# Performance work log

Measured on AMD Instinct MI355X. Metric: run time of the kernel, lower is better.

The kernel has to match this reference:

```python
import jax, jax.numpy as jnp
import numpy as np

N_NODES = 50000
N_EDGES = 800000
D_IN = 96
HID = 128


def _glorot(key, shape):
    fan_in, fan_out = shape[0], shape[1]
    lim = np.sqrt(6.0 / (fan_in + fan_out)).astype(np.float32)
    return jax.random.uniform(key, shape, jnp.float32, -lim, lim)


def setup_inputs() -> dict:
    key = jax.random.key(0)
    ks = jax.random.split(key, 12)
    x = jax.random.normal(ks[0], (N_NODES, D_IN), jnp.float32)
    edge_index = jax.random.randint(ks[1], (2, N_EDGES), 0, N_NODES)
    return {
        "x": x,
        "edge_index": edge_index,
        "W_in": _glorot(ks[2], (D_IN, HID)),
        "b_in": jnp.zeros((HID,), jnp.float32),
        "W1": _glorot(ks[3], (HID, HID)),
        "b1": jnp.zeros((HID,), jnp.float32),
        "W2": _glorot(ks[4], (HID, HID)),
        "b2": jnp.zeros((HID,), jnp.float32),
        "Wm1": _glorot(ks[5], (2 * HID, HID)),
        "bm1": jnp.zeros((HID,), jnp.float32),
        "Wm2": _glorot(ks[6], (HID, 1)),
        "bm2": jnp.zeros((1,), jnp.float32),
    }


def _gcn_conv(h, W, b, src, dst, n_nodes):
    # PyG GCNConv with add_self_loops=True, normalize=True:
    # out = D^{-1/2} (A + I) D^{-1/2} (h W) + b, aggregating x_j (source) into dst.
    loop = jnp.arange(n_nodes)
    row = jnp.concatenate([src, loop])  # source / j
    col = jnp.concatenate([dst, loop])  # target / i
    deg = jax.ops.segment_sum(jnp.ones(row.shape, h.dtype), col, num_segments=n_nodes)
    dinv = jnp.where(deg > 0, jax.lax.rsqrt(deg), 0.0)
    norm = dinv[row] * dinv[col]  # [E+N]
    xw = h @ W  # [N, H]
    msg = xw[row] * norm[:, None]  # gather + scale, [E+N, H]
    out = jax.ops.segment_sum(msg, col, num_segments=n_nodes)  # scatter-add
    return out + b


def reference(x, edge_index, W_in, b_in, W1, b1, W2, b2, Wm1, bm1, Wm2, bm2):
    src, dst = edge_index[0], edge_index[1]
    n = x.shape[0]
    h = jax.nn.relu(x @ W_in + b_in)  # dropout is identity at inference
    h = jax.nn.relu(_gcn_conv(h, W1, b1, src, dst, n))
    h = jax.nn.relu(_gcn_conv(h, W2, b2, src, dst, n))
    ef = jnp.concatenate([h[src], h[dst]], axis=1)  # [E, 2H]
    hid = jax.nn.relu(ef @ Wm1 + bm1)
    logits = (hid @ Wm2 + bm2)[:, 0]  # [E]
    return logits
```

## Files before the change

### kernel.cpp

```cpp
#include <hip/hip_runtime.h>

#define N_NODES 50000
#define N_EDGES 800000
#define D_IN 96
#define HID 128
#define NB 391
#define BCAP 3072

typedef __attribute__((ext_vector_type(8))) _Float16 halfx8;
typedef __attribute__((ext_vector_type(2))) _Float16 half2v;
typedef __attribute__((ext_vector_type(16))) float f32x16;


__global__ __launch_bounds__(256) void bucket_hist_kernel(const int* __restrict__ dst,
                                                          int* __restrict__ bhist) {
    __shared__ int lh[NB];
    int t = threadIdx.x;
    for (int i = t; i < NB; i += 256) lh[i] = 0;
    __syncthreads();
    int base = blockIdx.x * 4096;
#pragma unroll
    for (int i = 0; i < 16; i++) {
        int e = base + i * 256 + t;
        if (e < N_EDGES) atomicAdd(&lh[dst[e] >> 7], 1);
    }
    __syncthreads();
    for (int i = t; i < NB; i += 256) atomicAdd(&bhist[i], lh[i]);
}

__global__ __launch_bounds__(512) void scan_buckets_kernel(const int* __restrict__ bhist,
                                                           int* __restrict__ boff,
                                                           int* __restrict__ bcursor) {
    __shared__ int s[512];
    int t = threadIdx.x;
    int v = (t < NB) ? bhist[t] : 0;
    s[t] = v;
    __syncthreads();
    for (int off = 1; off < 512; off <<= 1) {
        int u = (t >= off) ? s[t - off] : 0;
        __syncthreads();
        s[t] += u;
        __syncthreads();
    }
    if (t < NB) {
        int ex = s[t] - v;
        boff[t] = ex;
        bcursor[t] = ex;
    }
    if (t == NB - 1) boff[NB] = s[t];
}

__global__ __launch_bounds__(512) void bin_kernel(const int* __restrict__ src,
                                                  const int* __restrict__ dst,
                                                  int* __restrict__ bcursor,
                                                  unsigned long long* __restrict__ binned) {
    __shared__ int lh[NB];
    __shared__ int gbs[NB];
    int t = threadIdx.x;
    for (int i = t; i < NB; i += 512) lh[i] = 0;
    __syncthreads();
    int base = blockIdx.x * 8192;
    unsigned long long pk[16];
    int bb[16], rk[16];
#pragma unroll
    for (int i = 0; i < 16; i++) {
        int e = base + i * 512 + t;
        bb[i] = -1;
        if (e < N_EDGES) {
            int s = src[e], d = dst[e];
            int b = d >> 7;
            bb[i] = b;
            pk[i] = ((unsigned long long)s << 27) |
                    ((unsigned long long)(d & 127) << 20) | (unsigned long long)e;
            rk[i] = atomicAdd(&lh[b], 1);
        }
    }
    __syncthreads();
    for (int i = t; i < NB; i += 512) gbs[i] = atomicAdd(&bcursor[i], lh[i]);
    __syncthreads();
#pragma unroll
    for (int i = 0; i < 16; i++) {
        if (bb[i] >= 0) binned[gbs[bb[i]] + rk[i]] = pk[i];
    }
}

__global__ __launch_bounds__(256) void bucket_sort_kernel(const unsigned long long* __restrict__ binned,
                                                          const int* __restrict__ boff,
                                                          int2* __restrict__ ce_se,
                                                          int* __restrict__ ce_dst,
                                                          int* __restrict__ csr_ptr,
                                                          float* __restrict__ dinv) {
    __shared__ unsigned long long ed[BCAP];
    __shared__ int2 sorted[BCAP];
    __shared__ int cntA[128], sc[128];
    int b = blockIdx.x;
    int t = threadIdx.x;
    int base = boff[b];
    int k = boff[b + 1] - base;
    if (k > BCAP) k = BCAP;
    if (t < 128) { cntA[t] = 0; }
    __syncthreads();
    int rk[12], li[12];
    int nmine = 0;
    for (int i = t; i < k; i += 256) {
        unsigned long long p = binned[base + i];
        ed[i] = p;
        int d = (int)((p >> 20) & 127);
        rk[nmine] = atomicAdd(&cntA[d], 1);
        li[nmine] = i;
        nmine++;
    }
    __syncthreads();
    if (t < 128) sc[t] = cntA[t];
    __syncthreads();
    for (int off = 1; off < 128; off <<= 1) {
        int u = 0;
        if (t < 128 && t >= off) u = sc[t - off];
        __syncthreads();
        if (t < 128) sc[t] += u;
        __syncthreads();
    }
    for (int m = 0; m < nmine; m++) {
        unsigned long long p = ed[li[m]];
        int d = (int)((p >> 20) & 127);
        int pos = sc[d] - cntA[d] + rk[m];
        int srcn = (int)(p >> 27);
        int eid = (int)(p & 0xFFFFF);
        sorted[pos] = make_int2(srcn | (d << 16), eid);
    }
    __syncthreads();
    for (int i = t; i < k; i += 256) {
        int2 se = sorted[i];
        ce_se[base + i] = make_int2(se.x & 0xFFFF, se.y);
        ce_dst[base + i] = (b << 7) + (se.x >> 16);
    }
    if (t < 128) {
        int node = (b << 7) + t;
        if (node < N_NODES) {
            csr_ptr[node] = base + sc[t] - cntA[t];
            dinv[node] = 1.0f / sqrtf((float)(cntA[t] + 1));
        }
    }
    if (b == NB - 1 && t == 0) csr_ptr[N_NODES] = boff[NB];
}

__global__ __launch_bounds__(256) void convert_x_kernel(const float* __restrict__ x,
                                                        _Float16* __restrict__ xh, int n4) {
    int i = blockIdx.x * 256 + threadIdx.x;
    if (i < n4) {
        float4 v = ((const float4*)x)[i];
        half2v a = {(_Float16)v.x, (_Float16)v.y};
        half2v b = {(_Float16)v.z, (_Float16)v.w};
        ((half2v*)xh)[i * 2] = a;
        ((half2v*)xh)[i * 2 + 1] = b;
    }
}

__global__ __launch_bounds__(256) void pack_weights_kernel(const float* __restrict__ W_in,
                                                           const float* __restrict__ W1,
                                                           const float* __restrict__ W2,
                                                           const float* __restrict__ Wm1,
                                                           _Float16* __restrict__ packed) {
    int t = blockIdx.x * 256 + threadIdx.x;
    const float* Wsrc;
    int K, u;
    if (t < 12288)      { Wsrc = W_in;            K = 96;  u = t; }
    else if (t < 28672) { Wsrc = W1;              K = 128; u = t - 12288; }
    else if (t < 45056) { Wsrc = W2;              K = 128; u = t - 28672; }
    else if (t < 61440) { Wsrc = Wm1;             K = 128; u = t - 45056; }
    else                { Wsrc = Wm1 + 128 * 128; K = 128; u = t - 61440; }
    if (t >= 77824) return;
    int steps = K >> 4;
    int cb = u / (steps * 512);
    int rem = u - cb * steps * 512;
    int s = rem >> 9;
    int lane = (rem >> 3) & 63;
    int j = rem & 7;
    int k = s * 16 + ((lane >> 5) << 3) + j;
    int n = (cb << 5) + (lane & 31);
    packed[t] = (_Float16)Wsrc[k * 128 + n];
}

__global__ __launch_bounds__(256) void gemm_f16_kernel(const _Float16* __restrict__ A,
                                                       const _Float16* __restrict__ Wp,
                                                       const float* __restrict__ bias,
                                                       const float* __restrict__ rowscale,
                                                       _Float16* __restrict__ out,
                                                       int M, int K, int steps, int dorelu) {
    __shared__ _Float16 As[64 * 136];
    int tid = threadIdx.x;
    int M0 = blockIdx.x * 64;
    int stride = K + 8;
    int CH = K >> 3;
    int tot = 64 * CH;
    for (int i = tid; i < tot; i += 256) {
        int r = i / CH, c = i - r * CH;
        uint4 v = make_uint4(0, 0, 0, 0);
        int row = M0 + r;
        if (row < M) v = *(const uint4*)&A[(size_t)row * K + c * 8];
        *(uint4*)&As[r * stride + c * 8] = v;
    }
    __syncthreads();

    int wave = tid >> 6, lane = tid & 63;
    int rb = wave & 1;
    int cb0 = (wave >> 1) * 2;
    const halfx8* bp0 = (const halfx8*)Wp + (size_t)cb0 * steps * 64 + lane;
    const halfx8* bp1 = bp0 + (size_t)steps * 64;
    const _Float16* arow = &As[(rb * 32 + (lane & 31)) * stride + ((lane >> 5) << 3)];
    f32x16 acc0 = {}, acc1 = {};
    for (int s = 0; s < steps; s++) {
        halfx8 a = *(const halfx8*)&arow[s * 16];
        halfx8 b0 = bp0[s * 64];
        halfx8 b1 = bp1[s * 64];
        acc0 = __builtin_amdgcn_mfma_f32_32x32x16_f16(a, b0, acc0, 0, 0, 0);
        acc1 = __builtin_amdgcn_mfma_f32_32x32x16_f16(a, b1, acc1, 0, 0, 0);
    }

    int colA = cb0 * 32 + (lane & 31);
    int colB = colA + 32;
    float bA = bias ? bias[colA] : 0.f;
    float bB = bias ? bias[colB] : 0.f;
#pragma unroll
    for (int r = 0; r < 16; r++) {
        int rl = (r & 3) + 8 * (r >> 2) + 4 * (lane >> 5);
        int grow = M0 + rb * 32 + rl;
        if (grow < M) {
            float sc = rowscale ? rowscale[grow] : 1.f;
            float v0 = (acc0[r] + bA) * sc;
            float v1 = (acc1[r] + bB) * sc;
            if (dorelu) { v0 = fmaxf(v0, 0.f); v1 = fmaxf(v1, 0.f); }
            out[(size_t)grow * 128 + colA] = (_Float16)v0;
            out[(size_t)grow * 128 + colB] = (_Float16)v1;
        }
    }
}

__global__ __launch_bounds__(256) void gemm_uv_kernel(const _Float16* __restrict__ A,
                                                      const _Float16* __restrict__ WpU,
                                                      const _Float16* __restrict__ WpV,
                                                      const float* __restrict__ bm1,
                                                      _Float16* __restrict__ U,
                                                      _Float16* __restrict__ V,
                                                      int M) {
    const int K = 128, steps = 8;
    __shared__ _Float16 As[64 * 136];
    int tid = threadIdx.x;
    int M0 = blockIdx.x * 64;
    int stride = K + 8;
    for (int i = tid; i < 64 * 16; i += 256) {
        int r = i >> 4, c = i & 15;
        uint4 v = make_uint4(0, 0, 0, 0);
        int row = M0 + r;
        if (row < M) v = *(const uint4*)&A[(size_t)row * K + c * 8];
        *(uint4*)&As[r * stride + c * 8] = v;
    }
    __syncthreads();

    int wave = tid >> 6, lane = tid & 63;
    int rb = wave & 1;
    int cb0 = (wave >> 1) * 2;
    const halfx8* bu0 = (const halfx8*)WpU + (size_t)cb0 * steps * 64 + lane;
    const halfx8* bu1 = bu0 + (size_t)steps * 64;
    const halfx8* bv0 = (const halfx8*)WpV + (size_t)cb0 * steps * 64 + lane;
    const halfx8* bv1 = bv0 + (size_t)steps * 64;
    const _Float16* arow = &As[(rb * 32 + (lane & 31)) * stride + ((lane >> 5) << 3)];
    f32x16 au0 = {}, au1 = {}, av0 = {}, av1 = {};
    for (int s = 0; s < steps; s++) {
        halfx8 a = *(const halfx8*)&arow[s * 16];
        au0 = __builtin_amdgcn_mfma_f32_32x32x16_f16(a, bu0[s * 64], au0, 0, 0, 0);
        au1 = __builtin_amdgcn_mfma_f32_32x32x16_f16(a, bu1[s * 64], au1, 0, 0, 0);
        av0 = __builtin_amdgcn_mfma_f32_32x32x16_f16(a, bv0[s * 64], av0, 0, 0, 0);
        av1 = __builtin_amdgcn_mfma_f32_32x32x16_f16(a, bv1[s * 64], av1, 0, 0, 0);
    }

    int colA = cb0 * 32 + (lane & 31);
    int colB = colA + 32;
    float bA = bm1[colA], bB = bm1[colB];
#pragma unroll
    for (int r = 0; r < 16; r++) {
        int rl = (r & 3) + 8 * (r >> 2) + 4 * (lane >> 5);
        int grow = M0 + rb * 32 + rl;
        if (grow < M) {
            U[(size_t)grow * 128 + colA] = (_Float16)(au0[r] + bA);
            U[(size_t)grow * 128 + colB] = (_Float16)(au1[r] + bB);
            V[(size_t)grow * 128 + colA] = (_Float16)av0[r];
            V[(size_t)grow * 128 + colB] = (_Float16)av1[r];
        }
    }
}

__global__ __launch_bounds__(256) void aggregate_kernel(const _Float16* __restrict__ y,
                                                        const float* __restrict__ dinv,
                                                        const int* __restrict__ ptr,
                                                        const int2* __restrict__ ce_se,
                                                        const float* __restrict__ bias,
                                                        _Float16* __restrict__ out) {
    int node = blockIdx.x * 4 + (threadIdx.x >> 6);
    int lane = threadIdx.x & 63;
    int c = lane * 2;
    float di = dinv[node];
    half2v self = ((const half2v*)&y[(size_t)node * 128])[lane];
    float a0 = (float)self.x, a1 = (float)self.y;
    float b0 = 0.f, b1 = 0.f, c0 = 0.f, c1 = 0.f, d0 = 0.f, d1 = 0.f;
    int s0 = ptr[node], s1 = ptr[node + 1];
    int j = s0;
    for (; j + 7 < s1; j += 8) {
        int n0 = ce_se[j].x, n1 = ce_se[j + 1].x, n2 = ce_se[j + 2].x, n3 = ce_se[j + 3].x;
        int n4 = ce_se[j + 4].x, n5 = ce_se[j + 5].x, n6 = ce_se[j + 6].x, n7 = ce_se[j + 7].x;
        half2v v0 = ((const half2v*)&y[(size_t)n0 * 128])[lane];
        half2v v1 = ((const half2v*)&y[(size_t)n1 * 128])[lane];
        half2v v2 = ((const half2v*)&y[(size_t)n2 * 128])[lane];
        half2v v3 = ((const half2v*)&y[(size_t)n3 * 128])[lane];
        half2v v4 = ((const half2v*)&y[(size_t)n4 * 128])[lane];
        half2v v5 = ((const half2v*)&y[(size_t)n5 * 128])[lane];
        half2v v6 = ((const half2v*)&y[(size_t)n6 * 128])[lane];
        half2v v7 = ((const half2v*)&y[(size_t)n7 * 128])[lane];
        a0 += (float)v0.x + (float)v4.x; a1 += (float)v0.y + (float)v4.y;
        b0 += (float)v1.x + (float)v5.x; b1 += (float)v1.y + (float)v5.y;
        c0 += (float)v2.x + (float)v6.x; c1 += (float)v2.y + (float)v6.y;
        d0 += (float)v3.x + (float)v7.x; d1 += (float)v3.y + (float)v7.y;
    }
    for (; j < s1; j++) {
        int n = ce_se[j].x;
        half2v v = ((const half2v*)&y[(size_t)n * 128])[lane];
        a0 += (float)v.x; a1 += (float)v.y;
    }
    float2 bv = *(const float2*)&bias[c];
    float o0 = fmaxf(di * (a0 + b0 + c0 + d0) + bv.x, 0.f);
    float o1 = fmaxf(di * (a1 + b1 + c1 + d1) + bv.y, 0.f);
    half2v ov = {(_Float16)o0, (_Float16)o1};
    ((half2v*)&out[(size_t)node * 128])[lane] = ov;
}

__global__ __launch_bounds__(256) void edge_mlp_kernel(const _Float16* __restrict__ Ub,
                                                       const _Float16* __restrict__ Vb,
                                                       const int2* __restrict__ ce_se,
                                                       const int* __restrict__ ce_dst,
                                                       const float* __restrict__ Wm2,
                                                       const float* __restrict__ bm2,
                                                       float* __restrict__ out) {
    __shared__ int ssrc[32], sdst[32], seid[32];
    int tid = threadIdx.x;
    int e0 = blockIdx.x * 32;
    if (tid < 32) {
        int2 se = ce_se[e0 + tid];
        ssrc[tid] = se.x;
        seid[tid] = se.y;
    } else if (tid < 64) {
        sdst[tid - 32] = ce_dst[e0 + tid - 32];
    }
    __syncthreads();
    int g = tid >> 4;
    int l = tid & 15;
    int g2 = g + 16;
    halfx8 u0 = *(const halfx8*)&Ub[(size_t)ssrc[g] * 128 + l * 8];
    halfx8 v0 = *(const halfx8*)&Vb[(size_t)sdst[g] * 128 + l * 8];
    halfx8 u1 = *(const halfx8*)&Ub[(size_t)ssrc[g2] * 128 + l * 8];
    halfx8 v1 = *(const halfx8*)&Vb[(size_t)sdst[g2] * 128 + l * 8];
    float4 w0 = *(const float4*)&Wm2[l * 8];
    float4 w1 = *(const float4*)&Wm2[l * 8 + 4];
    float wm[8] = {w0.x, w0.y, w0.z, w0.w, w1.x, w1.y, w1.z, w1.w};
    float p0 = 0.f, p1 = 0.f;
#pragma unroll
    for (int t = 0; t < 8; t++) {
        p0 = fmaf(fmaxf((float)u0[t] + (float)v0[t], 0.f), wm[t], p0);
        p1 = fmaf(fmaxf((float)u1[t] + (float)v1[t], 0.f), wm[t], p1);
    }
    p0 += __shfl_xor(p0, 1); p1 += __shfl_xor(p1, 1);
    p0 += __shfl_xor(p0, 2); p1 += __shfl_xor(p1, 2);
    p0 += __shfl_xor(p0, 4); p1 += __shfl_xor(p1, 4);
    p0 += __shfl_xor(p0, 8); p1 += __shfl_xor(p1, 8);
    if (l == 0) {
        float bb = bm2[0];
        out[seid[g]] = p0 + bb;
        out[seid[g2]] = p1 + bb;
    }
}

extern "C" void kernel_launch(void* const* d_in, const int* in_sizes, int n_in,
                              void* d_out, int out_size, void* d_ws, size_t ws_size,
                              hipStream_t stream) {
    const float* x    = (const float*)d_in[0];
    const int* eidx   = (const int*)d_in[1];
    const float* W_in = (const float*)d_in[2];
    const float* b_in = (const float*)d_in[3];
    const float* W1   = (const float*)d_in[4];
    const float* b1   = (const float*)d_in[5];
    const float* W2   = (const float*)d_in[6];
    const float* b2   = (const float*)d_in[7];
    const float* Wm1  = (const float*)d_in[8];
    const float* bm1  = (const float*)d_in[9];
    const float* Wm2  = (const float*)d_in[10];
    const float* bm2  = (const float*)d_in[11];
    float* out = (float*)d_out;
    const int* src = eidx;
    const int* dst = eidx + N_EDGES;

    char* w = (char*)d_ws;
    size_t off = 0;
    auto alloc = [&](size_t bytes) -> char* {
        char* p = w + off;
        off = (off + bytes + 255) & ~(size_t)255;
        return p;
    };
    int* bhist    = (int*)alloc((size_t)NB * 4);
    int* boff     = (int*)alloc((size_t)(NB + 1) * 4);
    int* bcursor  = (int*)alloc((size_t)NB * 4);
    int* csr_ptr  = (int*)alloc((size_t)(N_NODES + 1) * 4);
    float* dinv   = (float*)alloc((size_t)N_NODES * 4);
    unsigned long long* binned = (unsigned long long*)alloc((size_t)N_EDGES * 8);
    int2* ce_se   = (int2*)alloc((size_t)N_EDGES * 8);
    int* ce_dst   = (int*)alloc((size_t)N_EDGES * 4);
    _Float16* xh  = (_Float16*)alloc((size_t)N_NODES * D_IN * 2);
    _Float16* Wp  = (_Float16*)alloc((size_t)77824 * 2);
    _Float16* hbuf = (_Float16*)alloc((size_t)N_NODES * HID * 2);
    _Float16* ybuf = (_Float16*)alloc((size_t)N_NODES * HID * 2);
    _Float16* Ub  = (_Float16*)alloc((size_t)N_NODES * HID * 2);
    _Float16* Vb  = (_Float16*)alloc((size_t)N_NODES * HID * 2);

    const _Float16* WpIn  = Wp;
    const _Float16* Wp1   = Wp + 12288;
    const _Float16* Wp2   = Wp + 28672;
    const _Float16* WpM1a = Wp + 45056;
    const _Float16* WpM1b = Wp + 61440;

    hipMemsetAsync(bhist, 0, (size_t)NB * 4, stream);
    bucket_hist_kernel<<<196, 256, 0, stream>>>(dst, bhist);
    scan_buckets_kernel<<<1, 512, 0, stream>>>(bhist, boff, bcursor);
    bin_kernel<<<98, 512, 0, stream>>>(src, dst, bcursor, binned);
    bucket_sort_kernel<<<NB, 256, 0, stream>>>(binned, boff, ce_se, ce_dst, csr_ptr, dinv);

    convert_x_kernel<<<(N_NODES * D_IN / 4 + 255) / 256, 256, 0, stream>>>(
        x, xh, N_NODES * D_IN / 4);
    pack_weights_kernel<<<(77824 + 255) / 256, 256, 0, stream>>>(W_in, W1, W2, Wm1, Wp);

    int gblocks = (N_NODES + 63) / 64;
    gemm_f16_kernel<<<gblocks, 256, 0, stream>>>(xh, WpIn, b_in, nullptr, hbuf,
                                                 N_NODES, D_IN, 6, 1);
    gemm_f16_kernel<<<gblocks, 256, 0, stream>>>(hbuf, Wp1, nullptr, dinv, ybuf,
                                                 N_NODES, HID, 8, 0);
    aggregate_kernel<<<N_NODES / 4, 256, 0, stream>>>(ybuf, dinv, csr_ptr, ce_se, b1, hbuf);
    gemm_f16_kernel<<<gblocks, 256, 0, stream>>>(hbuf, Wp2, nullptr, dinv, ybuf,
                                                 N_NODES, HID, 8, 0);
    aggregate_kernel<<<N_NODES / 4, 256, 0, stream>>>(ybuf, dinv, csr_ptr, ce_se, b2, hbuf);
    gemm_uv_kernel<<<gblocks, 256, 0, stream>>>(hbuf, WpM1a, WpM1b, bm1, Ub, Vb, N_NODES);
    edge_mlp_kernel<<<N_EDGES / 32, 256, 0, stream>>>(Ub, Vb, ce_se, ce_dst, Wm2, bm2, out);
}
```

Before: 297.0 us.

## Fuse input conversion with GEMMs and aggregation with following GEMM

Folds the fp32-to-fp16 conversion of x into the input GEMM and chains the W_in and W1 products in one kernel through shared memory. Each GCN aggregation now writes its 64-node tile into shared memory and immediately runs the next dense GEMM (W2, or the U/V projections). This removes the intermediate h round-trips to global memory and several launches. The edge MLP kernel also handles 64 edges per block instead of 32. The trade-off is that the aggregation phase now runs with only 782 blocks walking 16 nodes each serially, which lowers parallelism for the gather-bound part.

```diff
diff --git a/kernel.cpp b/kernel.cpp
--- a/kernel.cpp
+++ b/kernel.cpp
@@ -10,7 +10,6 @@
 typedef __attribute__((ext_vector_type(8))) _Float16 halfx8;
 typedef __attribute__((ext_vector_type(2))) _Float16 half2v;
 typedef __attribute__((ext_vector_type(16))) float f32x16;
-
 
 __global__ __launch_bounds__(256) void bucket_hist_kernel(const int* __restrict__ dst,
                                                           int* __restrict__ bhist) {
@@ -98,7 +97,7 @@
     int base = boff[b];
     int k = boff[b + 1] - base;
     if (k > BCAP) k = BCAP;
-    if (t < 128) { cntA[t] = 0; }
+    if (t < 128) cntA[t] = 0;
     __syncthreads();
     int rk[12], li[12];
     int nmine = 0;
@@ -142,18 +141,6 @@
         }
     }
     if (b == NB - 1 && t == 0) csr_ptr[N_NODES] = boff[NB];
-}
-
-__global__ __launch_bounds__(256) void convert_x_kernel(const float* __restrict__ x,
-                                                        _Float16* __restrict__ xh, int n4) {
-    int i = blockIdx.x * 256 + threadIdx.x;
-    if (i < n4) {
-        float4 v = ((const float4*)x)[i];
-        half2v a = {(_Float16)v.x, (_Float16)v.y};
-        half2v b = {(_Float16)v.z, (_Float16)v.w};
-        ((half2v*)xh)[i * 2] = a;
-        ((half2v*)xh)[i * 2 + 1] = b;
-    }
 }
 
 __global__ __launch_bounds__(256) void pack_weights_kernel(const float* __restrict__ W_in,
@@ -181,156 +168,185 @@
     packed[t] = (_Float16)Wsrc[k * 128 + n];
 }
 
-__global__ __launch_bounds__(256) void gemm_f16_kernel(const _Float16* __restrict__ A,
-                                                       const _Float16* __restrict__ Wp,
-                                                       const float* __restrict__ bias,
-                                                       const float* __restrict__ rowscale,
-                                                       _Float16* __restrict__ out,
-                                                       int M, int K, int steps, int dorelu) {
-    __shared__ _Float16 As[64 * 136];
+__global__ __launch_bounds__(256) void fused_in_kernel(const float* __restrict__ x,
+                                                       const _Float16* __restrict__ WpIn,
+                                                       const _Float16* __restrict__ Wp1,
+                                                       const float* __restrict__ b_in,
+                                                       const float* __restrict__ dinv,
+                                                       _Float16* __restrict__ y1, int M) {
+    __shared__ _Float16 As[64 * 104];
+    __shared__ _Float16 Hs[64 * 136];
     int tid = threadIdx.x;
     int M0 = blockIdx.x * 64;
-    int stride = K + 8;
-    int CH = K >> 3;
-    int tot = 64 * CH;
-    for (int i = tid; i < tot; i += 256) {
-        int r = i / CH, c = i - r * CH;
-        uint4 v = make_uint4(0, 0, 0, 0);
+    for (int i = tid; i < 64 * 24; i += 256) {
+        int r = i / 24, c = i - r * 24;
+        float4 v = make_float4(0.f, 0.f, 0.f, 0.f);
         int row = M0 + r;
-        if (row < M) v = *(const uint4*)&A[(size_t)row * K + c * 8];
-        *(uint4*)&As[r * stride + c * 8] = v;
+        if (row < M) v = *(const float4*)&x[(size_t)row * 96 + c * 4];
+        half2v a = {(_Float16)v.x, (_Float16)v.y};
+        half2v b = {(_Float16)v.z, (_Float16)v.w};
+        *(half2v*)&As[r * 104 + c * 4] = a;
+        *(half2v*)&As[r * 104 + c * 4 + 2] = b;
     }
     __syncthreads();
 
     int wave = tid >> 6, lane = tid & 63;
     int rb = wave & 1;
     int cb0 = (wave >> 1) * 2;
-    const halfx8* bp0 = (const halfx8*)Wp + (size_t)cb0 * steps * 64 + lane;
-    const halfx8* bp1 = bp0 + (size_t)steps * 64;
-    const _Float16* arow = &As[(rb * 32 + (lane & 31)) * stride + ((lane >> 5) << 3)];
-    f32x16 acc0 = {}, acc1 = {};
-    for (int s = 0; s < steps; s++) {
-        halfx8 a = *(const halfx8*)&arow[s * 16];
-        halfx8 b0 = bp0[s * 64];
-        halfx8 b1 = bp1[s * 64];
-        acc0 = __builtin_amdgcn_mfma_f32_32x32x16_f16(a, b0, acc0, 0, 0, 0);
-        acc1 = __builtin_amdgcn_mfma_f32_32x32x16_f16(a, b1, acc1, 0, 0, 0);
-    }
-
     int colA = cb0 * 32 + (lane & 31);
     int colB = colA + 32;
-    float bA = bias ? bias[colA] : 0.f;
-    float bB = bias ? bias[colB] : 0.f;
-#pragma unroll
-    for (int r = 0; r < 16; r++) {
-        int rl = (r & 3) + 8 * (r >> 2) + 4 * (lane >> 5);
-        int grow = M0 + rb * 32 + rl;
-        if (grow < M) {
-            float sc = rowscale ? rowscale[grow] : 1.f;
-            float v0 = (acc0[r] + bA) * sc;
-            float v1 = (acc1[r] + bB) * sc;
-            if (dorelu) { v0 = fmaxf(v0, 0.f); v1 = fmaxf(v1, 0.f); }
-            out[(size_t)grow * 128 + colA] = (_Float16)v0;
-            out[(size_t)grow * 128 + colB] = (_Float16)v1;
-        }
-    }
-}
-
-__global__ __launch_bounds__(256) void gemm_uv_kernel(const _Float16* __restrict__ A,
-                                                      const _Float16* __restrict__ WpU,
-                                                      const _Float16* __restrict__ WpV,
-                                                      const float* __restrict__ bm1,
-                                                      _Float16* __restrict__ U,
-                                                      _Float16* __restrict__ V,
-                                                      int M) {
-    const int K = 128, steps = 8;
-    __shared__ _Float16 As[64 * 136];
+    {
+        const halfx8* bp0 = (const halfx8*)WpIn + (size_t)cb0 * 6 * 64 + lane;
+        const halfx8* bp1 = bp0 + (size_t)6 * 64;
+        const _Float16* arow = &As[(rb * 32 + (lane & 31)) * 104 + ((lane >> 5) << 3)];
+        f32x16 acc0 = {}, acc1 = {};
+#pragma unroll
+        for (int s = 0; s < 6; s++) {
+            halfx8 a = *(const halfx8*)&arow[s * 16];
+            acc0 = __builtin_amdgcn_mfma_f32_32x32x16_f16(a, bp0[s * 64], acc0, 0, 0, 0);
+            acc1 = __builtin_amdgcn_mfma_f32_32x32x16_f16(a, bp1[s * 64], acc1, 0, 0, 0);
+        }
+        float bA = b_in[colA], bB = b_in[colB];
+#pragma unroll
+        for (int r = 0; r < 16; r++) {
+            int rl = (r & 3) + 8 * (r >> 2) + 4 * (lane >> 5);
+            int lrow = rb * 32 + rl;
+            Hs[lrow * 136 + colA] = (_Float16)fmaxf(acc0[r] + bA, 0.f);
+            Hs[lrow * 136 + colB] = (_Float16)fmaxf(acc1[r] + bB, 0.f);
+        }
+    }
+    __syncthreads();
+    {
+        const halfx8* bp0 = (const halfx8*)Wp1 + (size_t)cb0 * 8 * 64 + lane;
+        const halfx8* bp1 = bp0 + (size_t)8 * 64;
+        const _Float16* arow = &Hs[(rb * 32 + (lane & 31)) * 136 + ((lane >> 5) << 3)];
+        f32x16 acc0 = {}, acc1 = {};
+#pragma unroll
+        for (int s = 0; s < 8; s++) {
+            halfx8 a = *(const halfx8*)&arow[s * 16];
+            acc0 = __builtin_amdgcn_mfma_f32_32x32x16_f16(a, bp0[s * 64], acc0, 0, 0, 0);
+            acc1 = __builtin_amdgcn_mfma_f32_32x32x16_f16(a, bp1[s * 64], acc1, 0, 0, 0);
+        }
+#pragma unroll
+        for (int r = 0; r < 16; r++) {
+            int rl = (r & 3) + 8 * (r >> 2) + 4 * (lane >> 5);
+            int grow = M0 + rb * 32 + rl;
+            if (grow < M) {
+                float sc = dinv[grow];
+                y1[(size_t)grow * 128 + colA] = (_Float16)(acc0[r] * sc);
+                y1[(size_t)grow * 128 + colB] = (_Float16)(acc1[r] * sc);
+            }
+        }
+    }
+}
+
+__global__ __launch_bounds__(256) void fused_agg_gemm_kernel(
+    const _Float16* __restrict__ y, const float* __restrict__ dinv,
+    const int* __restrict__ ptr, const int2* __restrict__ ce_se,
+    const float* __restrict__ aggbias,
+    const _Float16* __restrict__ WpA, const float* __restrict__ biasA, int useRS,
+    const _Float16* __restrict__ WpB,
+    _Float16* __restrict__ outA, _Float16* __restrict__ outB, int M) {
+    __shared__ _Float16 Hs[64 * 136];
     int tid = threadIdx.x;
     int M0 = blockIdx.x * 64;
-    int stride = K + 8;
-    for (int i = tid; i < 64 * 16; i += 256) {
-        int r = i >> 4, c = i & 15;
-        uint4 v = make_uint4(0, 0, 0, 0);
-        int row = M0 + r;
-        if (row < M) v = *(const uint4*)&A[(size_t)row * K + c * 8];
-        *(uint4*)&As[r * stride + c * 8] = v;
-    }
-    __syncthreads();
-
     int wave = tid >> 6, lane = tid & 63;
+    int c = lane * 2;
+    float2 bv = *(const float2*)&aggbias[c];
+
+    for (int pass = 0; pass < 16; pass++) {
+        int ln = pass * 4 + wave;
+        int node = M0 + ln;
+        float o0 = 0.f, o1 = 0.f;
+        if (node < M) {
+            float di = dinv[node];
+            half2v self = ((const half2v*)&y[(size_t)node * 128])[lane];
+            float a0 = (float)self.x, a1 = (float)self.y;
+            float b0 = 0.f, b1 = 0.f, c0 = 0.f, c1 = 0.f, d0 = 0.f, d1 = 0.f;
+            int s0 = ptr[node], s1 = ptr[node + 1];
+            int j = s0;
+            for (; j + 7 < s1; j += 8) {
+                int n0 = ce_se[j].x, n1 = ce_se[j + 1].x, n2 = ce_se[j + 2].x, n3 = ce_se[j + 3].x;
+                int n4 = ce_se[j + 4].x, n5 = ce_se[j + 5].x, n6 = ce_se[j + 6].x, n7 = ce_se[j + 7].x;
+                half2v v0 = ((const half2v*)&y[(size_t)n0 * 128])[lane];
+                half2v v1 = ((const half2v*)&y[(size_t)n1 * 128])[lane];
+                half2v v2 = ((const half2v*)&y[(size_t)n2 * 128])[lane];
+                half2v v3 = ((const half2v*)&y[(size_t)n3 * 128])[lane];
+                half2v v4 = ((const half2v*)&y[(size_t)n4 * 128])[lane];
+                half2v v5 = ((const half2v*)&y[(size_t)n5 * 128])[lane];
+                half2v v6 = ((const half2v*)&y[(size_t)n6 * 128])[lane];
+                half2v v7 = ((const half2v*)&y[(size_t)n7 * 128])[lane];
+                a0 += (float)v0.x + (float)v4.x; a1 += (float)v0.y + (float)v4.y;
+                b0 += (float)v1.x + (float)v5.x; b1 += (float)v1.y + (float)v5.y;
+                c0 += (float)v2.x + (float)v6.x; c1 += (float)v2.y + (float)v6.y;
+                d0 += (float)v3.x + (float)v7.x; d1 += (float)v3.y + (float)v7.y;
+            }
+            for (; j < s1; j++) {
+                int n = ce_se[j].x;
+                half2v v = ((const half2v*)&y[(size_t)n * 128])[lane];
+                a0 += (float)v.x; a1 += (float)v.y;
+            }
+            o0 = fmaxf(di * (a0 + b0 + c0 + d0) + bv.x, 0.f);
+            o1 = fmaxf(di * (a1 + b1 + c1 + d1) + bv.y, 0.f);
+        }
+        half2v ov = {(_Float16)o0, (_Float16)o1};
+        *(half2v*)&Hs[ln * 136 + c] = ov;
+    }
+    __syncthreads();
+
     int rb = wave & 1;
     int cb0 = (wave >> 1) * 2;
-    const halfx8* bu0 = (const halfx8*)WpU + (size_t)cb0 * steps * 64 + lane;
-    const halfx8* bu1 = bu0 + (size_t)steps * 64;
-    const halfx8* bv0 = (const halfx8*)WpV + (size_t)cb0 * steps * 64 + lane;
-    const halfx8* bv1 = bv0 + (size_t)steps * 64;
-    const _Float16* arow = &As[(rb * 32 + (lane & 31)) * stride + ((lane >> 5) << 3)];
-    f32x16 au0 = {}, au1 = {}, av0 = {}, av1 = {};
-    for (int s = 0; s < steps; s++) {
-        halfx8 a = *(const halfx8*)&arow[s * 16];
-        au0 = __builtin_amdgcn_mfma_f32_32x32x16_f16(a, bu0[s * 64], au0, 0, 0, 0);
-        au1 = __builtin_amdgcn_mfma_f32_32x32x16_f16(a, bu1[s * 64], au1, 0, 0, 0);
-        av0 = __builtin_amdgcn_mfma_f32_32x32x16_f16(a, bv0[s * 64], av0, 0, 0, 0);
-        av1 = __builtin_amdgcn_mfma_f32_32x32x16_f16(a, bv1[s * 64], av1, 0, 0, 0);
-    }
-
     int colA = cb0 * 32 + (lane & 31);
     int colB = colA + 32;
-    float bA = bm1[colA], bB = bm1[colB];
-#pragma unroll
-    for (int r = 0; r < 16; r++) {
-        int rl = (r & 3) + 8 * (r >> 2) + 4 * (lane >> 5);
-        int grow = M0 + rb * 32 + rl;
-        if (grow < M) {
-            U[(size_t)grow * 128 + colA] = (_Float16)(au0[r] + bA);
-            U[(size_t)grow * 128 + colB] = (_Float16)(au1[r] + bB);
-            V[(size_t)grow * 128 + colA] = (_Float16)av0[r];
-            V[(size_t)grow * 128 + colB] = (_Float16)av1[r];
-        }
-    }
-}
-
-__global__ __launch_bounds__(256) void aggregate_kernel(const _Float16* __restrict__ y,
-                                                        const float* __restrict__ dinv,
-                                                        const int* __restrict__ ptr,
-                                                        const int2* __restrict__ ce_se,
-                                                        const float* __restrict__ bias,
-                                                        _Float16* __restrict__ out) {
-    int node = blockIdx.x * 4 + (threadIdx.x >> 6);
-    int lane = threadIdx.x & 63;
-    int c = lane * 2;
-    float di = dinv[node];
-    half2v self = ((const half2v*)&y[(size_t)node * 128])[lane];
-    float a0 = (float)self.x, a1 = (float)self.y;
-    float b0 = 0.f, b1 = 0.f, c0 = 0.f, c1 = 0.f, d0 = 0.f, d1 = 0.f;
-    int s0 = ptr[node], s1 = ptr[node + 1];
-    int j = s0;
-    for (; j + 7 < s1; j += 8) {
-        int n0 = ce_se[j].x, n1 = ce_se[j + 1].x, n2 = ce_se[j + 2].x, n3 = ce_se[j + 3].x;
-        int n4 = ce_se[j + 4].x, n5 = ce_se[j + 5].x, n6 = ce_se[j + 6].x, n7 = ce_se[j + 7].x;
-        half2v v0 = ((const half2v*)&y[(size_t)n0 * 128])[lane];
-        half2v v1 = ((const half2v*)&y[(size_t)n1 * 128])[lane];
-        half2v v2 = ((const half2v*)&y[(size_t)n2 * 128])[lane];
-        half2v v3 = ((const half2v*)&y[(size_t)n3 * 128])[lane];
-        half2v v4 = ((const half2v*)&y[(size_t)n4 * 128])[lane];
-        half2v v5 = ((const half2v*)&y[(size_t)n5 * 128])[lane];
-        half2v v6 = ((const half2v*)&y[(size_t)n6 * 128])[lane];
-        half2v v7 = ((const half2v*)&y[(size_t)n7 * 128])[lane];
-        a0 += (float)v0.x + (float)v4.x; a1 += (float)v0.y + (float)v4.y;
-        b0 += (float)v1.x + (float)v5.x; b1 += (float)v1.y + (float)v5.y;
-        c0 += (float)v2.x + (float)v6.x; c1 += (float)v2.y + (float)v6.y;
-        d0 += (float)v3.x + (float)v7.x; d1 += (float)v3.y + (float)v7.y;
-    }
-    for (; j < s1; j++) {
-        int n = ce_se[j].x;
-        half2v v = ((const half2v*)&y[(size_t)n * 128])[lane];
-        a0 += (float)v.x; a1 += (float)v.y;
-    }
-    float2 bv = *(const float2*)&bias[c];
-    float o0 = fmaxf(di * (a0 + b0 + c0 + d0) + bv.x, 0.f);
-    float o1 = fmaxf(di * (a1 + b1 + c1 + d1) + bv.y, 0.f);
-    half2v ov = {(_Float16)o0, (_Float16)o1};
-    ((half2v*)&out[(size_t)node * 128])[lane] = ov;
+    const _Float16* arow = &Hs[(rb * 32 + (lane & 31)) * 136 + ((lane >> 5) << 3)];
+    const halfx8* ba0 = (const halfx8*)WpA + (size_t)cb0 * 8 * 64 + lane;
+    const halfx8* ba1 = ba0 + (size_t)8 * 64;
+    f32x16 aa0 = {}, aa1 = {};
+    if (outB) {
+        const halfx8* bb0 = (const halfx8*)WpB + (size_t)cb0 * 8 * 64 + lane;
+        const halfx8* bb1 = bb0 + (size_t)8 * 64;
+        f32x16 ab0 = {}, ab1 = {};
+#pragma unroll
+        for (int s = 0; s < 8; s++) {
+            halfx8 a = *(const halfx8*)&arow[s * 16];
+            aa0 = __builtin_amdgcn_mfma_f32_32x32x16_f16(a, ba0[s * 64], aa0, 0, 0, 0);
+            aa1 = __builtin_amdgcn_mfma_f32_32x32x16_f16(a, ba1[s * 64], aa1, 0, 0, 0);
+            ab0 = __builtin_amdgcn_mfma_f32_32x32x16_f16(a, bb0[s * 64], ab0, 0, 0, 0);
+            ab1 = __builtin_amdgcn_mfma_f32_32x32x16_f16(a, bb1[s * 64], ab1, 0, 0, 0);
+        }
+        float bA = biasA ? biasA[colA] : 0.f;
+        float bB = biasA ? biasA[colB] : 0.f;
+#pragma unroll
+        for (int r = 0; r < 16; r++) {
+            int rl = (r & 3) + 8 * (r >> 2) + 4 * (lane >> 5);
+            int grow = M0 + rb * 32 + rl;
+            if (grow < M) {
+                outA[(size_t)grow * 128 + colA] = (_Float16)(aa0[r] + bA);
+                outA[(size_t)grow * 128 + colB] = (_Float16)(aa1[r] + bB);
+                outB[(size_t)grow * 128 + colA] = (_Float16)ab0[r];
+                outB[(size_t)grow * 128 + colB] = (_Float16)ab1[r];
+            }
+        }
+    } else {
+#pragma unroll
+        for (int s = 0; s < 8; s++) {
+            halfx8 a = *(const halfx8*)&arow[s * 16];
+            aa0 = __builtin_amdgcn_mfma_f32_32x32x16_f16(a, ba0[s * 64], aa0, 0, 0, 0);
+            aa1 = __builtin_amdgcn_mfma_f32_32x32x16_f16(a, ba1[s * 64], aa1, 0, 0, 0);
+        }
+        float bA = biasA ? biasA[colA] : 0.f;
+        float bB = biasA ? biasA[colB] : 0.f;
+#pragma unroll
+        for (int r = 0; r < 16; r++) {
+            int rl = (r & 3) + 8 * (r >> 2) + 4 * (lane >> 5);
+            int grow = M0 + rb * 32 + rl;
+            if (grow < M) {
+                float sc = useRS ? dinv[grow] : 1.f;
+                outA[(size_t)grow * 128 + colA] = (_Float16)((aa0[r] + bA) * sc);
+                outA[(size_t)grow * 128 + colB] = (_Float16)((aa1[r] + bB) * sc);
+            }
+        }
+    }
 }
 
 __global__ __launch_bounds__(256) void edge_mlp_kernel(const _Float16* __restrict__ Ub,
@@ -340,41 +356,52 @@
                                                        const float* __restrict__ Wm2,
                                                        const float* __restrict__ bm2,
                                                        float* __restrict__ out) {
-    __shared__ int ssrc[32], sdst[32], seid[32];
+    __shared__ int ssrc[64], sdst[64], seid[64];
     int tid = threadIdx.x;
-    int e0 = blockIdx.x * 32;
-    if (tid < 32) {
+    int e0 = blockIdx.x * 64;
+    if (tid < 64) {
         int2 se = ce_se[e0 + tid];
         ssrc[tid] = se.x;
         seid[tid] = se.y;
-    } else if (tid < 64) {
-        sdst[tid - 32] = ce_dst[e0 + tid - 32];
+    } else if (tid < 128) {
+        sdst[tid - 64] = ce_dst[e0 + tid - 64];
     }
     __syncthreads();
     int g = tid >> 4;
     int l = tid & 15;
-    int g2 = g + 16;
-    halfx8 u0 = *(const halfx8*)&Ub[(size_t)ssrc[g] * 128 + l * 8];
-    halfx8 v0 = *(const halfx8*)&Vb[(size_t)sdst[g] * 128 + l * 8];
-    halfx8 u1 = *(const halfx8*)&Ub[(size_t)ssrc[g2] * 128 + l * 8];
-    halfx8 v1 = *(const halfx8*)&Vb[(size_t)sdst[g2] * 128 + l * 8];
+    int ga = g, gb = g + 16, gc = g + 32, gd = g + 48;
+    halfx8 u0 = *(const halfx8*)&Ub[(size_t)ssrc[ga] * 128 + l * 8];
+    halfx8 v0 = *(const halfx8*)&Vb[(size_t)sdst[ga] * 128 + l * 8];
+    halfx8 u1 = *(const halfx8*)&Ub[(size_t)ssrc[gb] * 128 + l * 8];
+    halfx8 v1 = *(const halfx8*)&Vb[(size_t)sdst[gb] * 128 + l * 8];
+    halfx8 u2 = *(const halfx8*)&Ub[(size_t)ssrc[gc] * 128 + l * 8];
+    halfx8 v2 = *(const halfx8*)&Vb[(size_t)sdst[gc] * 128 + l * 8];
+    halfx8 u3 = *(const halfx8*)&Ub[(size_t)ssrc[gd] * 128 + l * 8];
+    halfx8 v3 = *(const halfx8*)&Vb[(size_t)sdst[gd] * 128 + l * 8];
     float4 w0 = *(const float4*)&Wm2[l * 8];
     float4 w1 = *(const float4*)&Wm2[l * 8 + 4];
     float wm[8] = {w0.x, w0.y, w0.z, w0.w, w1.x, w1.y, w1.z, w1.w};
-    float p0 = 0.f, p1 = 0.f;
+    float p0 = 0.f, p1 = 0.f, p2 = 0.f, p3 = 0.f;
 #pragma unroll
     for (int t = 0; t < 8; t++) {
         p0 = fmaf(fmaxf((float)u0[t] + (float)v0[t], 0.f), wm[t], p0);
         p1 = fmaf(fmaxf((float)u1[t] + (float)v1[t], 0.f), wm[t], p1);
-    }
-    p0 += __shfl_xor(p0, 1); p1 += __shfl_xor(p1, 1);
-    p0 += __shfl_xor(p0, 2); p1 += __shfl_xor(p1, 2);
-    p0 += __shfl_xor(p0, 4); p1 += __shfl_xor(p1, 4);
-    p0 += __shfl_xor(p0, 8); p1 += __shfl_xor(p1, 8);
+        p2 = fmaf(fmaxf((float)u2[t] + (float)v2[t], 0.f), wm[t], p2);
+        p3 = fmaf(fmaxf((float)u3[t] + (float)v3[t], 0.f), wm[t], p3);
+    }
+#pragma unroll
+    for (int d = 1; d < 16; d <<= 1) {
+        p0 += __shfl_xor(p0, d);
+        p1 += __shfl_xor(p1, d);
+        p2 += __shfl_xor(p2, d);
+        p3 += __shfl_xor(p3, d);
+    }
     if (l == 0) {
         float bb = bm2[0];
-        out[seid[g]] = p0 + bb;
-        out[seid[g2]] = p1 + bb;
+        out[seid[ga]] = p0 + bb;
+        out[seid[gb]] = p1 + bb;
+        out[seid[gc]] = p2 + bb;
+        out[seid[gd]] = p3 + bb;
     }
 }
 
@@ -412,10 +439,9 @@
     unsigned long long* binned = (unsigned long long*)alloc((size_t)N_EDGES * 8);
     int2* ce_se   = (int2*)alloc((size_t)N_EDGES * 8);
     int* ce_dst   = (int*)alloc((size_t)N_EDGES * 4);
-    _Float16* xh  = (_Float16*)alloc((size_t)N_NODES * D_IN * 2);
     _Float16* Wp  = (_Float16*)alloc((size_t)77824 * 2);
-    _Float16* hbuf = (_Float16*)alloc((size_t)N_NODES * HID * 2);
-    _Float16* ybuf = (_Float16*)alloc((size_t)N_NODES * HID * 2);
+    _Float16* y1  = (_Float16*)alloc((size_t)N_NODES * HID * 2);
+    _Float16* y2  = (_Float16*)alloc((size_t)N_NODES * HID * 2);
     _Float16* Ub  = (_Float16*)alloc((size_t)N_NODES * HID * 2);
     _Float16* Vb  = (_Float16*)alloc((size_t)N_NODES * HID * 2);
 
@@ -430,20 +456,15 @@
     scan_buckets_kernel<<<1, 512, 0, stream>>>(bhist, boff, bcursor);
     bin_kernel<<<98, 512, 0, stream>>>(src, dst, bcursor, binned);
     bucket_sort_kernel<<<NB, 256, 0, stream>>>(binned, boff, ce_se, ce_dst, csr_ptr, dinv);
-
-    convert_x_kernel<<<(N_NODES * D_IN / 4 + 255) / 256, 256, 0, stream>>>(
-        x, xh, N_NODES * D_IN / 4);
     pack_weights_kernel<<<(77824 + 255) / 256, 256, 0, stream>>>(W_in, W1, W2, Wm1, Wp);
 
     int gblocks = (N_NODES + 63) / 64;
-    gemm_f16_kernel<<<gblocks, 256, 0, stream>>>(xh, WpIn, b_in, nullptr, hbuf,
-                                                 N_NODES, D_IN, 6, 1);
-    gemm_f16_kernel<<<gblocks, 256, 0, stream>>>(hbuf, Wp1, nullptr, dinv, ybuf,
-                                                 N_NODES, HID, 8, 0);
-    aggregate_kernel<<<N_NODES / 4, 256, 0, stream>>>(ybuf, dinv, csr_ptr, ce_se, b1, hbuf);
-    gemm_f16_kernel<<<gblocks, 256, 0, stream>>>(hbuf, Wp2, nullptr, dinv, ybuf,
-                                                 N_NODES, HID, 8, 0);
-    aggregate_kernel<<<N_NODES / 4, 256, 0, stream>>>(ybuf, dinv, csr_ptr, ce_se, b2, hbuf);
-    gemm_uv_kernel<<<gblocks, 256, 0, stream>>>(hbuf, WpM1a, WpM1b, bm1, Ub, Vb, N_NODES);
-    edge_mlp_kernel<<<N_EDGES / 32, 256, 0, stream>>>(Ub, Vb, ce_se, ce_dst, Wm2, bm2, out);
-}
+    fused_in_kernel<<<gblocks, 256, 0, stream>>>(x, WpIn, Wp1, b_in, dinv, y1, N_NODES);
+    fused_agg_gemm_kernel<<<gblocks, 256, 0, stream>>>(y1, dinv, csr_ptr, ce_se, b1,
+                                                       Wp2, nullptr, 1, nullptr,
+                                                       y2, nullptr, N_NODES);
+    fused_agg_gemm_kernel<<<gblocks, 256, 0, stream>>>(y2, dinv, csr_ptr, ce_se, b2,
+                                                       WpM1a, bm1, 0, WpM1b,
+                                                       Ub, Vb, N_NODES);
+    edge_mlp_kernel<<<N_EDGES / 64, 256, 0, stream>>>(Ub, Vb, ce_se, ce_dst, Wm2, bm2, out);
+}
```

Result: slower. 404.7 us (+36.3%).
